# Kernel optimization log

Measured on AMD Instinct MI355X. Metric: run time of the kernel, lower is better.

The kernel has to match this reference:

```python
import jax, jax.numpy as jnp
import numpy as np

N = 8192          # num_nodes (feature dim == node count, x is square)
H = N // 2        # hidden channels of conv1
NUM_GRAPHS = 8    # graphs in the batch for global_mean_pool
EDGE_P = 0.004    # adjacency density -> avg degree ~33


def setup_inputs() -> dict:
    key = jax.random.key(0)
    kx, kb, k1, k2 = jax.random.split(key, 4)
    # sparse binary adjacency-as-features: nonzero(x) defines the edge list
    x = (jax.random.uniform(kx, (N, N)) < EDGE_P).astype(jnp.float32)
    batch = jnp.sort(jax.random.randint(kb, (N,), 0, NUM_GRAPHS))
    # GCNConv weights (lin has no bias in PyG; separate additive bias)
    W1 = jax.random.normal(k1, (N, H), jnp.float32) / np.sqrt(N)
    b1 = jnp.zeros((H,), jnp.float32)
    W2 = jax.random.normal(k2, (H, N), jnp.float32) / np.sqrt(H)
    b2 = jnp.zeros((N,), jnp.float32)
    return {"x": x, "W1": W1, "b1": b1, "W2": W2, "b2": b2, "batch": batch}


def _gcn_norm_adj(x):
    """Symmetric-normalized adjacency implied by edge_index = nonzero(x).

    PyG GCNConv: edges (r -> c) for every nonzero x[r, c], unit edge weight,
    remaining self loops added, deg = in-degree of target, message to node c is
    deg^-1/2[r] * deg^-1/2[c] * xw[r]. Since x is square/dense we express the
    aggregation as a dense normalized-adjacency matmul (identical math).
    """
    A = (x != 0).astype(x.dtype)                # [N, N], A[r, c] = edge r->c
    idx = jnp.arange(A.shape[0])
    A = A.at[idx, idx].set(1.0)                 # add (remaining) self loops
    deg = A.sum(axis=0)                         # in-degree of each target node
    dinv = jax.lax.rsqrt(deg)                   # deg >= 1 (self loops)
    return dinv[:, None] * A * dinv[None, :]    # B[r, c] = dinv[r]*A[r,c]*dinv[c]


def reference(x, W1, b1, W2, b2, batch):
    B = _gcn_norm_adj(x)
    # conv1: aggregate_c sum_r B[r, c] * (x @ W1)[r]  == B.T @ (x @ W1)
    h = jax.nn.relu(B.T @ (x @ W1) + b1)        # [N, H]
    h = B.T @ (h @ W2) + b2                     # [N, N]
    # global_mean_pool over graph assignment `batch`
    sums = jax.ops.segment_sum(h, batch, num_segments=NUM_GRAPHS)
    cnt = jax.ops.segment_sum(jnp.ones((h.shape[0],), h.dtype), batch,
                              num_segments=NUM_GRAPHS)
    return sums / jnp.maximum(cnt, 1.0)[:, None]  # [NUM_GRAPHS, N]
```

## Files before the change

kernel.cpp:

```cpp
#include <hip/hip_runtime.h>
#include <hip/hip_bf16.h>

#define NN 8192
#define HH 4096
#define GG 8
#define STR 128
#define NCH 32
#define CHU 16
#define PRG 64
#define FJG 32

typedef unsigned uint4n __attribute__((ext_vector_type(4)));

__device__ inline unsigned bf16rne(float f) {
    unsigned u = __float_as_uint(f);
    unsigned r = 0x7fffu + ((u >> 16) & 1u);
    return (u + r) >> 16;
}
__device__ inline unsigned pack2(float lo, float hi) {
    return bf16rne(lo) | (bf16rne(hi) << 16);
}
__device__ inline void nt_store16(void* p, unsigned a, unsigned b, unsigned c, unsigned d) {
    uint4n v; v.x = a; v.y = b; v.z = c; v.w = d;
    __builtin_nontemporal_store(v, reinterpret_cast<uint4n*>(p));
}
__device__ inline void acc8p(float2* __restrict__ acc2, uint4 v) {
    const unsigned* pu = reinterpret_cast<const unsigned*>(&v);
    #pragma unroll
    for (int q = 0; q < 4; ++q) {
        const unsigned u = pu[q];
        float2 t;
        t.x = __uint_as_float(u << 16);
        t.y = __uint_as_float(u & 0xffff0000u);
        asm("v_pk_add_f32 %0, %1, %0" : "+v"(acc2[q]) : "v"(t));
    }
}
__device__ inline void unpack8(uint4 v, float* __restrict__ h) {
    const unsigned* pu = reinterpret_cast<const unsigned*>(&v);
    #pragma unroll
    for (int q = 0; q < 4; ++q) {
        const unsigned u = pu[q];
        h[2 * q]     = __uint_as_float(u << 16);
        h[2 * q + 1] = __uint_as_float(u & 0xffff0000u);
    }
}

__global__ __launch_bounds__(256) void k_cvt(const float* __restrict__ src,
                                             uint4* __restrict__ dst) {
    const size_t i = (size_t)blockIdx.x * 256 + threadIdx.x;
    const float4 a = reinterpret_cast<const float4*>(src)[2 * i];
    const float4 b = reinterpret_cast<const float4*>(src)[2 * i + 1];
    nt_store16(&dst[i], pack2(a.x, a.y), pack2(a.z, a.w),
                        pack2(b.x, b.y), pack2(b.z, b.w));
}

__global__ __launch_bounds__(256) void k_build(const float* __restrict__ x,
                                               unsigned* __restrict__ colfill,
                                               unsigned* __restrict__ degX,
                                               unsigned* __restrict__ degA,
                                               unsigned* __restrict__ csrX,
                                               unsigned* __restrict__ csrA,
                                               unsigned* __restrict__ cscA) {
    const int r = blockIdx.x;
    __shared__ unsigned px, pa;
    if (threadIdx.x == 0) { px = 0u; pa = 0u; }
    __syncthreads();
    const float4* xr = reinterpret_cast<const float4*>(x + (size_t)r * NN);
    #pragma unroll
    for (int i = 0; i < NN / (4 * 256); ++i) {
        const int c4 = i * 256 + threadIdx.x;
        float4 v = xr[c4];
        const float* vp = reinterpret_cast<const float*>(&v);
        #pragma unroll
        for (int k = 0; k < 4; ++k) {
            const int c = c4 * 4 + k;
            const bool nzx = (vp[k] != 0.0f);
            const bool nzA = nzx || (c == r);
            if (nzx) {
                unsigned p = atomicAdd(&px, 1u);
                if (p < STR) csrX[(size_t)r * STR + p] = (unsigned)c << 13;
            }
            if (nzA) {
                unsigned p = atomicAdd(&pa, 1u);
                if (p < STR) csrA[(size_t)r * STR + p] = (unsigned)c;
                unsigned q = atomicAdd(&colfill[c], 1u);
                if (q < STR) cscA[(size_t)c * STR + q] = (unsigned)r << 13;
            }
        }
    }
    __syncthreads();
    if (threadIdx.x == 0) { degX[r] = px; degA[r] = pa; }
}

__global__ __launch_bounds__(256) void k_prep(const unsigned* __restrict__ colfill,
                                              const int* __restrict__ batch,
                                              float* __restrict__ dinv,
                                              unsigned* __restrict__ cnt) {
    const int i = blockIdx.x * 256 + threadIdx.x;
    dinv[i] = rsqrtf((float)colfill[i]);
    atomicAdd(&cnt[batch[i]], 1u);
}

__global__ __launch_bounds__(256) void k_s(const unsigned* __restrict__ degA,
                                           const unsigned* __restrict__ csrA,
                                           const float* __restrict__ dinv,
                                           const int* __restrict__ batch,
                                           float* __restrict__ s) {
    const int r = blockIdx.x * 256 + threadIdx.x;
    unsigned deg = degA[r];
    if (deg > STR) deg = STR;
    float bins[GG];
    #pragma unroll
    for (int g = 0; g < GG; ++g) bins[g] = 0.0f;
    for (unsigned e = 0; e < deg; ++e) {
        const unsigned c = csrA[(size_t)r * STR + e];
        const float d = dinv[c];
        const int gb = batch[c];
        #pragma unroll
        for (int g = 0; g < GG; ++g) bins[g] += (gb == g) ? d : 0.0f;
    }
    const float dr = dinv[r];
    #pragma unroll
    for (int g = 0; g < GG; ++g) s[(size_t)g * NN + r] = dr * bins[g];
}

__global__ __launch_bounds__(256) void k_spmm1(const char* __restrict__ W1b,
                                               const unsigned* __restrict__ degX,
                                               const unsigned* __restrict__ csrX,
                                               const float* __restrict__ dinv,
                                               uint4* __restrict__ Mh) {
    const unsigned L = blockIdx.x;
    const int xcd   = L & 7;
    const unsigned k = L >> 3;
    const int phase = k >> 11;
    const int pix   = k & 2047;
    const int ch    = xcd + (phase << 3);
    const int wid   = threadIdx.x >> 6;
    const int lane  = threadIdx.x & 63;
    const int node  = (pix << 2) | wid;
    const int sub   = lane >> 4;
    const int l16   = lane & 15;
    __shared__ unsigned offs[4][STR];
    unsigned deg = degX[node];
    if (deg > STR) deg = STR;
    for (unsigned i = lane; i < deg; i += 64)
        offs[wid][i] = csrX[(size_t)node * STR + i];
    __syncthreads();

    const unsigned loff = (unsigned)(ch * CHU + l16) * 16u;
    float2 acc2[4];
    #pragma unroll
    for (int q = 0; q < 4; ++q) acc2[q] = make_float2(0.f, 0.f);
    unsigned e = sub;
    for (; e + 12 < deg; e += 16) {
        const uint4 v0 = *reinterpret_cast<const uint4*>(W1b + (offs[wid][e]      + loff));
        const uint4 v1 = *reinterpret_cast<const uint4*>(W1b + (offs[wid][e + 4]  + loff));
        const uint4 v2 = *reinterpret_cast<const uint4*>(W1b + (offs[wid][e + 8]  + loff));
        const uint4 v3 = *reinterpret_cast<const uint4*>(W1b + (offs[wid][e + 12] + loff));
        acc8p(acc2, v0); acc8p(acc2, v1); acc8p(acc2, v2); acc8p(acc2, v3);
    }
    for (; e < deg; e += 4)
        acc8p(acc2, *reinterpret_cast<const uint4*>(W1b + (offs[wid][e] + loff)));

    #pragma unroll
    for (int q = 0; q < 4; ++q) {
        acc2[q].x += __shfl_xor(acc2[q].x, 16);
        acc2[q].y += __shfl_xor(acc2[q].y, 16);
        acc2[q].x += __shfl_xor(acc2[q].x, 32);
        acc2[q].y += __shfl_xor(acc2[q].y, 32);
    }
    if (sub == 0) {
        const float dr = dinv[node];
        nt_store16(&Mh[(size_t)node * (HH / 8) + ch * CHU + l16],
                   pack2(dr * acc2[0].x, dr * acc2[0].y),
                   pack2(dr * acc2[1].x, dr * acc2[1].y),
                   pack2(dr * acc2[2].x, dr * acc2[2].y),
                   pack2(dr * acc2[3].x, dr * acc2[3].y));
    }
}

__global__ __launch_bounds__(256) void k_conv1(const char* __restrict__ Mb,
                                               const float* __restrict__ b1,
                                               const float* __restrict__ dinv,
                                               const unsigned* __restrict__ colfill,
                                               const unsigned* __restrict__ cscA,
                                               uint4* __restrict__ hB) {
    const unsigned L = blockIdx.x;
    const int xcd   = L & 7;
    const unsigned k = L >> 3;
    const int phase = k >> 11;
    const int pix   = k & 2047;
    const int ch    = xcd + (phase << 3);
    const int wid   = threadIdx.x >> 6;
    const int lane  = threadIdx.x & 63;
    const int node  = (pix << 2) | wid;
    const int sub   = lane >> 4;
    const int l16   = lane & 15;
    __shared__ unsigned offs[4][STR];
    unsigned deg = colfill[node];
    if (deg > STR) deg = STR;
    for (unsigned i = lane; i < deg; i += 64)
        offs[wid][i] = cscA[(size_t)node * STR + i];
    __syncthreads();

    const unsigned loff = (unsigned)(ch * CHU + l16) * 16u;
    float2 acc2[4];
    #pragma unroll
    for (int q = 0; q < 4; ++q) acc2[q] = make_float2(0.f, 0.f);
    unsigned e = sub;
    for (; e + 12 < deg; e += 16) {
        const uint4 v0 = *reinterpret_cast<const uint4*>(Mb + (offs[wid][e]      + loff));
        const uint4 v1 = *reinterpret_cast<const uint4*>(Mb + (offs[wid][e + 4]  + loff));
        const uint4 v2 = *reinterpret_cast<const uint4*>(Mb + (offs[wid][e + 8]  + loff));
        const uint4 v3 = *reinterpret_cast<const uint4*>(Mb + (offs[wid][e + 12] + loff));
        acc8p(acc2, v0); acc8p(acc2, v1); acc8p(acc2, v2); acc8p(acc2, v3);
    }
    for (; e < deg; e += 4)
        acc8p(acc2, *reinterpret_cast<const uint4*>(Mb + (offs[wid][e] + loff)));

    #pragma unroll
    for (int q = 0; q < 4; ++q) {
        acc2[q].x += __shfl_xor(acc2[q].x, 16);
        acc2[q].y += __shfl_xor(acc2[q].y, 16);
        acc2[q].x += __shfl_xor(acc2[q].x, 32);
        acc2[q].y += __shfl_xor(acc2[q].y, 32);
    }
    if (sub == 0) {
        const float dc = dinv[node];
        const float4 ba = reinterpret_cast<const float4*>(b1)[ch * (CHU * 2) + l16 * 2];
        const float4 bb = reinterpret_cast<const float4*>(b1)[ch * (CHU * 2) + l16 * 2 + 1];
        float h[8];
        h[0] = fmaxf(fmaf(dc, acc2[0].x, ba.x), 0.0f);
        h[1] = fmaxf(fmaf(dc, acc2[0].y, ba.y), 0.0f);
        h[2] = fmaxf(fmaf(dc, acc2[1].x, ba.z), 0.0f);
        h[3] = fmaxf(fmaf(dc, acc2[1].y, ba.w), 0.0f);
        h[4] = fmaxf(fmaf(dc, acc2[2].x, bb.x), 0.0f);
        h[5] = fmaxf(fmaf(dc, acc2[2].y, bb.y), 0.0f);
        h[6] = fmaxf(fmaf(dc, acc2[3].x, bb.z), 0.0f);
        h[7] = fmaxf(fmaf(dc, acc2[3].y, bb.w), 0.0f);
        nt_store16(&hB[(size_t)node * (HH / 8) + ch * CHU + l16],
                   pack2(h[0], h[1]), pack2(h[2], h[3]),
                   pack2(h[4], h[5]), pack2(h[6], h[7]));
    }
}

__global__ __launch_bounds__(256) void k_poolA(const uint4* __restrict__ hB,
                                               const float* __restrict__ s,
                                               float* __restrict__ part) {
    const int j = blockIdx.x * 256 + threadIdx.x;
    const int c0 = blockIdx.y * (NN / PRG);
    __shared__ float s_t[GG * (NN / PRG)];
    for (int i = threadIdx.x; i < GG * (NN / PRG); i += 256) {
        const int g = i / (NN / PRG);
        const int cc = i % (NN / PRG);
        s_t[i] = s[(size_t)g * NN + c0 + cc];
    }
    __syncthreads();
    float tacc[GG][8];
    #pragma unroll
    for (int g = 0; g < GG; ++g)
        #pragma unroll
        for (int q = 0; q < 8; ++q) tacc[g][q] = 0.0f;
    for (int cc = 0; cc < NN / PRG; ++cc) {
        const uint4 v = hB[(size_t)(c0 + cc) * (HH / 8) + j];
        float hv[8];
        unpack8(v, hv);
        #pragma unroll
        for (int g = 0; g < GG; ++g) {
            const float sv = s_t[g * (NN / PRG) + cc];
            #pragma unroll
            for (int q = 0; q < 8; ++q) tacc[g][q] = fmaf(sv, hv[q], tacc[g][q]);
        }
    }
    float4* p4 = reinterpret_cast<float4*>(part);
    #pragma unroll
    for (int g = 0; g < GG; ++g) {
        const size_t base = ((size_t)(blockIdx.y * GG + g) * HH) / 4 + j * 2;
        p4[base]     = make_float4(tacc[g][0], tacc[g][1], tacc[g][2], tacc[g][3]);
        p4[base + 1] = make_float4(tacc[g][4], tacc[g][5], tacc[g][6], tacc[g][7]);
    }
}

__global__ __launch_bounds__(256) void k_poolB(const float* __restrict__ part,
                                               float* __restrict__ t) {
    const int idx = blockIdx.x * 256 + threadIdx.x;
    const int g = idx / (HH / 4);
    const int j4 = idx % (HH / 4);
    const float4* p4 = reinterpret_cast<const float4*>(part);
    float4 acc = make_float4(0.f, 0.f, 0.f, 0.f);
    for (int rg = 0; rg < PRG; ++rg) {
        const float4 v = p4[((size_t)(rg * GG + g) * HH) / 4 + j4];
        acc.x += v.x; acc.y += v.y; acc.z += v.z; acc.w += v.w;
    }
    reinterpret_cast<float4*>(t)[idx] = acc;
}

__global__ __launch_bounds__(256) void k_final(const float* __restrict__ W2,
                                               const float* __restrict__ t,
                                               const unsigned* __restrict__ cnt,
                                               float* __restrict__ part2) {
    __shared__ float tld[GG * 128];
    const int tj = threadIdx.x;
    const int j0 = blockIdx.y * 128;
    const int nbase = blockIdx.x * 1024;
    for (int i = threadIdx.x; i < GG * 128; i += 256) {
        const int g = i >> 7;
        const int jj = i & 127;
        unsigned c = cnt[g];
        if (c < 1u) c = 1u;
        tld[i] = t[(size_t)g * HH + j0 + jj] * (1.0f / (float)c);
    }
    __syncthreads();
    float4 acc[GG];
    #pragma unroll
    for (int g = 0; g < GG; ++g) acc[g] = make_float4(0.f, 0.f, 0.f, 0.f);
    for (int jj = 0; jj < 128; ++jj) {
        const int jv = j0 + jj;
        float4 w = reinterpret_cast<const float4*>(W2 + (size_t)jv * NN + nbase)[tj];
        #pragma unroll
        for (int g = 0; g < GG; ++g) {
            const float tv = tld[g * 128 + jj];
            acc[g].x = fmaf(tv, w.x, acc[g].x);
            acc[g].y = fmaf(tv, w.y, acc[g].y);
            acc[g].z = fmaf(tv, w.z, acc[g].z);
            acc[g].w = fmaf(tv, w.w, acc[g].w);
        }
    }
    float4* p4 = reinterpret_cast<float4*>(part2);
    #pragma unroll
    for (int g = 0; g < GG; ++g)
        p4[((size_t)(blockIdx.y * GG + g) * NN + nbase) / 4 + tj] = acc[g];
}

__global__ __launch_bounds__(256) void k_fin2(const float* __restrict__ part2,
                                              const float* __restrict__ b2,
                                              float* __restrict__ out) {
    const int idx = blockIdx.x * 256 + threadIdx.x;
    const int g = idx / (NN / 4);
    const int n4 = idx % (NN / 4);
    const float4* p4 = reinterpret_cast<const float4*>(part2);
    float4 acc = reinterpret_cast<const float4*>(b2)[n4];
    for (int jg = 0; jg < FJG; ++jg) {
        const float4 v = p4[((size_t)(jg * GG + g) * NN) / 4 + n4];
        acc.x += v.x; acc.y += v.y; acc.z += v.z; acc.w += v.w;
    }
    reinterpret_cast<float4*>(out)[idx] = acc;
}

extern "C" void kernel_launch(void* const* d_in, const int* in_sizes, int n_in,
                              void* d_out, int out_size, void* d_ws, size_t ws_size,
                              hipStream_t stream) {
    const float* x  = (const float*)d_in[0];
    const float* W1 = (const float*)d_in[1];
    const float* b1 = (const float*)d_in[2];
    const float* W2 = (const float*)d_in[3];
    const float* b2 = (const float*)d_in[4];
    const int* batch = (const int*)d_in[5];
    float* out = (float*)d_out;

    char* ws = (char*)d_ws;
    size_t off = 0;
    auto alloc = [&](size_t bytes) -> char* {
        char* p = ws + off;
        off = (off + bytes + 255) & ~(size_t)255;
        return p;
    };
    uint4*    Mh      = (uint4*)   alloc((size_t)NN * HH * 2);
    uint4*    W1h     = (uint4*)   alloc((size_t)NN * HH * 2);
    uint4*    hB      = W1h;
    char*     zbegin  = ws + off;
    float*    t       = (float*)   alloc((size_t)GG * HH * 4);
    unsigned* colfill = (unsigned*)alloc((size_t)NN * 4);
    unsigned* cnt     = (unsigned*)alloc((size_t)GG * 4);
    char*     zend    = ws + off;
    float*    s       = (float*)   alloc((size_t)GG * NN * 4);
    float*    dinv    = (float*)   alloc((size_t)NN * 4);
    unsigned* degX    = (unsigned*)alloc((size_t)NN * 4);
    unsigned* degA    = (unsigned*)alloc((size_t)NN * 4);
    unsigned* csrX    = (unsigned*)alloc((size_t)NN * STR * 4);
    unsigned* csrA    = (unsigned*)alloc((size_t)NN * STR * 4);
    unsigned* cscA    = (unsigned*)alloc((size_t)NN * STR * 4);
    float*    part    = (float*)csrX;
    float*    part2   = (float*)csrX;
    (void)ws_size; (void)in_sizes; (void)n_in; (void)out_size;

    hipMemsetAsync(zbegin, 0, (size_t)(zend - zbegin), stream);

    k_cvt<<<(NN * HH / 8) / 256, 256, 0, stream>>>(W1, (uint4*)W1h);
    k_build<<<NN, 256, 0, stream>>>(x, colfill, degX, degA, csrX, csrA, cscA);
    k_prep<<<NN / 256, 256, 0, stream>>>(colfill, batch, dinv, cnt);
    k_s<<<NN / 256, 256, 0, stream>>>(degA, csrA, dinv, batch, s);
    k_spmm1<<<(NN / 4) * NCH, 256, 0, stream>>>((const char*)W1h, degX, csrX, dinv, Mh);
    k_conv1<<<(NN / 4) * NCH, 256, 0, stream>>>((const char*)Mh, b1, dinv, colfill, cscA, hB);
    k_poolA<<<dim3(HH / 2048, PRG), 256, 0, stream>>>(hB, s, part);
    k_poolB<<<(GG * HH / 4) / 256, 256, 0, stream>>>(part, t);
    k_final<<<dim3(NN / 1024, FJG), 256, 0, stream>>>(W2, t, cnt, part2);
    k_fin2<<<(GG * NN / 4) / 256, 256, 0, stream>>>(part2, b2, out);
}
```

Baseline: 634.7 us.

## Restructure sparse gathers to one wave per node with 4-byte lanes, no LDS

Both sparse aggregation kernels (x@W1 gather and the normalized-adjacency gather) now assign each wave a full 64-lane row chunk of 2 bf16 values per lane, so every lane walks the whole edge list itself. This removes the LDS staging of edge offsets, the block barrier and the cross-subgroup shuffle reduction. Edge indices are made wave-uniform via readfirstlane so they can be fetched through scalar loads, and the loop is unrolled by 8. The trade-off is narrower 4-byte per-lane gathers instead of 16-byte ones, and a longer serial edge loop per wave.

Result: no change. 640.1 us (+0.9%).

```diff
diff --git a/kernel.cpp b/kernel.cpp
--- a/kernel.cpp
+++ b/kernel.cpp
@@ -6,7 +6,6 @@
 #define GG 8
 #define STR 128
 #define NCH 32
-#define CHU 16
 #define PRG 64
 #define FJG 32
 
@@ -24,16 +23,11 @@
     uint4n v; v.x = a; v.y = b; v.z = c; v.w = d;
     __builtin_nontemporal_store(v, reinterpret_cast<uint4n*>(p));
 }
-__device__ inline void acc8p(float2* __restrict__ acc2, uint4 v) {
-    const unsigned* pu = reinterpret_cast<const unsigned*>(&v);
-    #pragma unroll
-    for (int q = 0; q < 4; ++q) {
-        const unsigned u = pu[q];
-        float2 t;
-        t.x = __uint_as_float(u << 16);
-        t.y = __uint_as_float(u & 0xffff0000u);
-        asm("v_pk_add_f32 %0, %1, %0" : "+v"(acc2[q]) : "v"(t));
-    }
+__device__ inline void acc2p(float2& acc, unsigned u) {
+    float2 t;
+    t.x = __uint_as_float(u << 16);
+    t.y = __uint_as_float(u & 0xffff0000u);
+    asm("v_pk_add_f32 %0, %1, %0" : "+v"(acc) : "v"(t));
 }
 __device__ inline void unpack8(uint4 v, float* __restrict__ h) {
     const unsigned* pu = reinterpret_cast<const unsigned*>(&v);
@@ -128,55 +122,46 @@
                                                const unsigned* __restrict__ degX,
                                                const unsigned* __restrict__ csrX,
                                                const float* __restrict__ dinv,
-                                               uint4* __restrict__ Mh) {
+                                               unsigned* __restrict__ Mh) {
     const unsigned L = blockIdx.x;
     const int xcd   = L & 7;
     const unsigned k = L >> 3;
     const int phase = k >> 11;
     const int pix   = k & 2047;
     const int ch    = xcd + (phase << 3);
-    const int wid   = threadIdx.x >> 6;
-    const int lane  = threadIdx.x & 63;
-    const int node  = (pix << 2) | wid;
-    const int sub   = lane >> 4;
-    const int l16   = lane & 15;
-    __shared__ unsigned offs[4][STR];
+    int node = (pix << 2) | (threadIdx.x >> 6);
+    node = __builtin_amdgcn_readfirstlane(node);
+    const int lane = threadIdx.x & 63;
+
     unsigned deg = degX[node];
     if (deg > STR) deg = STR;
-    for (unsigned i = lane; i < deg; i += 64)
-        offs[wid][i] = csrX[(size_t)node * STR + i];
-    __syncthreads();
-
-    const unsigned loff = (unsigned)(ch * CHU + l16) * 16u;
-    float2 acc2[4];
-    #pragma unroll
-    for (int q = 0; q < 4; ++q) acc2[q] = make_float2(0.f, 0.f);
-    unsigned e = sub;
-    for (; e + 12 < deg; e += 16) {
-        const uint4 v0 = *reinterpret_cast<const uint4*>(W1b + (offs[wid][e]      + loff));
-        const uint4 v1 = *reinterpret_cast<const uint4*>(W1b + (offs[wid][e + 4]  + loff));
-        const uint4 v2 = *reinterpret_cast<const uint4*>(W1b + (offs[wid][e + 8]  + loff));
-        const uint4 v3 = *reinterpret_cast<const uint4*>(W1b + (offs[wid][e + 12] + loff));
-        acc8p(acc2, v0); acc8p(acc2, v1); acc8p(acc2, v2); acc8p(acc2, v3);
-    }
-    for (; e < deg; e += 4)
-        acc8p(acc2, *reinterpret_cast<const uint4*>(W1b + (offs[wid][e] + loff)));
-
-    #pragma unroll
-    for (int q = 0; q < 4; ++q) {
-        acc2[q].x += __shfl_xor(acc2[q].x, 16);
-        acc2[q].y += __shfl_xor(acc2[q].y, 16);
-        acc2[q].x += __shfl_xor(acc2[q].x, 32);
-        acc2[q].y += __shfl_xor(acc2[q].y, 32);
-    }
-    if (sub == 0) {
-        const float dr = dinv[node];
-        nt_store16(&Mh[(size_t)node * (HH / 8) + ch * CHU + l16],
-                   pack2(dr * acc2[0].x, dr * acc2[0].y),
-                   pack2(dr * acc2[1].x, dr * acc2[1].y),
-                   pack2(dr * acc2[2].x, dr * acc2[2].y),
-                   pack2(dr * acc2[3].x, dr * acc2[3].y));
-    }
+    const unsigned* __restrict__ el = csrX + (size_t)node * STR;
+    const unsigned loff = (unsigned)(ch * 64 + lane) * 4u;
+
+    float2 acc = make_float2(0.f, 0.f);
+    unsigned e = 0;
+    for (; e + 8 <= deg; e += 8) {
+        unsigned o0 = el[e + 0], o1 = el[e + 1], o2 = el[e + 2], o3 = el[e + 3];
+        unsigned o4 = el[e + 4], o5 = el[e + 5], o6 = el[e + 6], o7 = el[e + 7];
+        const unsigned v0 = *reinterpret_cast<const unsigned*>(W1b + (o0 + loff));
+        const unsigned v1 = *reinterpret_cast<const unsigned*>(W1b + (o1 + loff));
+        const unsigned v2 = *reinterpret_cast<const unsigned*>(W1b + (o2 + loff));
+        const unsigned v3 = *reinterpret_cast<const unsigned*>(W1b + (o3 + loff));
+        const unsigned v4 = *reinterpret_cast<const unsigned*>(W1b + (o4 + loff));
+        const unsigned v5 = *reinterpret_cast<const unsigned*>(W1b + (o5 + loff));
+        const unsigned v6 = *reinterpret_cast<const unsigned*>(W1b + (o6 + loff));
+        const unsigned v7 = *reinterpret_cast<const unsigned*>(W1b + (o7 + loff));
+        acc2p(acc, v0); acc2p(acc, v1); acc2p(acc, v2); acc2p(acc, v3);
+        acc2p(acc, v4); acc2p(acc, v5); acc2p(acc, v6); acc2p(acc, v7);
+    }
+    for (; e < deg; ++e) {
+        unsigned o = el[e];
+        acc2p(acc, *reinterpret_cast<const unsigned*>(W1b + (o + loff)));
+    }
+
+    const float dr = dinv[node];
+    __builtin_nontemporal_store(pack2(dr * acc.x, dr * acc.y),
+                                &Mh[(size_t)node * (HH / 2) + ch * 64 + lane]);
 }
 
 __global__ __launch_bounds__(256) void k_conv1(const char* __restrict__ Mb,
@@ -184,64 +169,49 @@
                                                const float* __restrict__ dinv,
                                                const unsigned* __restrict__ colfill,
                                                const unsigned* __restrict__ cscA,
-                                               uint4* __restrict__ hB) {
+                                               unsigned* __restrict__ hB) {
     const unsigned L = blockIdx.x;
     const int xcd   = L & 7;
     const unsigned k = L >> 3;
     const int phase = k >> 11;
     const int pix   = k & 2047;
     const int ch    = xcd + (phase << 3);
-    const int wid   = threadIdx.x >> 6;
-    const int lane  = threadIdx.x & 63;
-    const int node  = (pix << 2) | wid;
-    const int sub   = lane >> 4;
-    const int l16   = lane & 15;
-    __shared__ unsigned offs[4][STR];
+    int node = (pix << 2) | (threadIdx.x >> 6);
+    node = __builtin_amdgcn_readfirstlane(node);
+    const int lane = threadIdx.x & 63;
+
     unsigned deg = colfill[node];
     if (deg > STR) deg = STR;
-    for (unsigned i = lane; i < deg; i += 64)
-        offs[wid][i] = cscA[(size_t)node * STR + i];
-    __syncthreads();
-
-    const unsigned loff = (unsigned)(ch * CHU + l16) * 16u;
-    float2 acc2[4];
-    #pragma unroll
-    for (int q = 0; q < 4; ++q) acc2[q] = make_float2(0.f, 0.f);
-    unsigned e = sub;
-    for (; e + 12 < deg; e += 16) {
-        const uint4 v0 = *reinterpret_cast<const uint4*>(Mb + (offs[wid][e]      + loff));
-        const uint4 v1 = *reinterpret_cast<const uint4*>(Mb + (offs[wid][e + 4]  + loff));
-        const uint4 v2 = *reinterpret_cast<const uint4*>(Mb + (offs[wid][e + 8]  + loff));
-        const uint4 v3 = *reinterpret_cast<const uint4*>(Mb + (offs[wid][e + 12] + loff));
-        acc8p(acc2, v0); acc8p(acc2, v1); acc8p(acc2, v2); acc8p(acc2, v3);
-    }
-    for (; e < deg; e += 4)
-        acc8p(acc2, *reinterpret_cast<const uint4*>(Mb + (offs[wid][e] + loff)));
-
-    #pragma unroll
-    for (int q = 0; q < 4; ++q) {
-        acc2[q].x += __shfl_xor(acc2[q].x, 16);
-        acc2[q].y += __shfl_xor(acc2[q].y, 16);
-        acc2[q].x += __shfl_xor(acc2[q].x, 32);
-        acc2[q].y += __shfl_xor(acc2[q].y, 32);
-    }
-    if (sub == 0) {
-        const float dc = dinv[node];
-        const float4 ba = reinterpret_cast<const float4*>(b1)[ch * (CHU * 2) + l16 * 2];
-        const float4 bb = reinterpret_cast<const float4*>(b1)[ch * (CHU * 2) + l16 * 2 + 1];
-        float h[8];
-        h[0] = fmaxf(fmaf(dc, acc2[0].x, ba.x), 0.0f);
-        h[1] = fmaxf(fmaf(dc, acc2[0].y, ba.y), 0.0f);
-        h[2] = fmaxf(fmaf(dc, acc2[1].x, ba.z), 0.0f);
-        h[3] = fmaxf(fmaf(dc, acc2[1].y, ba.w), 0.0f);
-        h[4] = fmaxf(fmaf(dc, acc2[2].x, bb.x), 0.0f);
-        h[5] = fmaxf(fmaf(dc, acc2[2].y, bb.y), 0.0f);
-        h[6] = fmaxf(fmaf(dc, acc2[3].x, bb.z), 0.0f);
-        h[7] = fmaxf(fmaf(dc, acc2[3].y, bb.w), 0.0f);
-        nt_store16(&hB[(size_t)node * (HH / 8) + ch * CHU + l16],
-                   pack2(h[0], h[1]), pack2(h[2], h[3]),
-                   pack2(h[4], h[5]), pack2(h[6], h[7]));
-    }
+    const unsigned* __restrict__ el = cscA + (size_t)node * STR;
+    const unsigned loff = (unsigned)(ch * 64 + lane) * 4u;
+
+    float2 acc = make_float2(0.f, 0.f);
+    unsigned e = 0;
+    for (; e + 8 <= deg; e += 8) {
+        unsigned o0 = el[e + 0], o1 = el[e + 1], o2 = el[e + 2], o3 = el[e + 3];
+        unsigned o4 = el[e + 4], o5 = el[e + 5], o6 = el[e + 6], o7 = el[e + 7];
+        const unsigned v0 = *reinterpret_cast<const unsigned*>(Mb + (o0 + loff));
+        const unsigned v1 = *reinterpret_cast<const unsigned*>(Mb + (o1 + loff));
+        const unsigned v2 = *reinterpret_cast<const unsigned*>(Mb + (o2 + loff));
+        const unsigned v3 = *reinterpret_cast<const unsigned*>(Mb + (o3 + loff));
+        const unsigned v4 = *reinterpret_cast<const unsigned*>(Mb + (o4 + loff));
+        const unsigned v5 = *reinterpret_cast<const unsigned*>(Mb + (o5 + loff));
+        const unsigned v6 = *reinterpret_cast<const unsigned*>(Mb + (o6 + loff));
+        const unsigned v7 = *reinterpret_cast<const unsigned*>(Mb + (o7 + loff));
+        acc2p(acc, v0); acc2p(acc, v1); acc2p(acc, v2); acc2p(acc, v3);
+        acc2p(acc, v4); acc2p(acc, v5); acc2p(acc, v6); acc2p(acc, v7);
+    }
+    for (; e < deg; ++e) {
+        unsigned o = el[e];
+        acc2p(acc, *reinterpret_cast<const unsigned*>(Mb + (o + loff)));
+    }
+
+    const float dc = dinv[node];
+    const float2 bv = reinterpret_cast<const float2*>(b1)[ch * 64 + lane];
+    const float h0 = fmaxf(fmaf(dc, acc.x, bv.x), 0.0f);
+    const float h1 = fmaxf(fmaf(dc, acc.y, bv.y), 0.0f);
+    __builtin_nontemporal_store(pack2(h0, h1),
+                                &hB[(size_t)node * (HH / 2) + ch * 64 + lane]);
 }
 
 __global__ __launch_bounds__(256) void k_poolA(const uint4* __restrict__ hB,
@@ -390,8 +360,10 @@
     k_build<<<NN, 256, 0, stream>>>(x, colfill, degX, degA, csrX, csrA, cscA);
     k_prep<<<NN / 256, 256, 0, stream>>>(colfill, batch, dinv, cnt);
     k_s<<<NN / 256, 256, 0, stream>>>(degA, csrA, dinv, batch, s);
-    k_spmm1<<<(NN / 4) * NCH, 256, 0, stream>>>((const char*)W1h, degX, csrX, dinv, Mh);
-    k_conv1<<<(NN / 4) * NCH, 256, 0, stream>>>((const char*)Mh, b1, dinv, colfill, cscA, hB);
+    k_spmm1<<<(NN / 4) * NCH, 256, 0, stream>>>((const char*)W1h, degX, csrX, dinv,
+                                                (unsigned*)Mh);
+    k_conv1<<<(NN / 4) * NCH, 256, 0, stream>>>((const char*)Mh, b1, dinv, colfill, cscA,
+                                                (unsigned*)hB);
     k_poolA<<<dim3(HH / 2048, PRG), 256, 0, stream>>>(hB, s, part);
     k_poolB<<<(GG * HH / 4) / 256, 256, 0, stream>>>(part, t);
     k_final<<<dim3(NN / 1024, FJG), 256, 0, stream>>>(W2, t, cnt, part2);
```
